# Kernel optimization log

Measured on AMD Instinct MI355X. Metric: run time of the kernel, lower is better.

The kernel has to match this reference:

```python
import jax, jax.numpy as jnp
import numpy as np

EPS = 1e-5
SCALE = 4


def _conv(x, w, b=None, stride=1, pad=0):
    y = jax.lax.conv_general_dilated(
        x, w, (stride, stride), ((pad, pad), (pad, pad)),
        dimension_numbers=("NCHW", "OIHW", "NCHW"))
    if b is not None:
        y = y + b[None, :, None, None]
    return y


def _bn(x, g, b, m, v):
    # inference-mode BatchNorm2d with running stats
    scale = g / jnp.sqrt(v + EPS)
    return (x - m[None, :, None, None]) * scale[None, :, None, None] + b[None, :, None, None]


def setup_inputs() -> dict:
    key = jax.random.key(0)
    ks = jax.random.split(key, 20)
    B, H, W = 2, 112, 256
    d = {}
    d["patch"] = jax.random.normal(ks[0], (B, 3, SCALE * H, SCALE * W), jnp.float32)
    d["disp"] = jax.random.normal(ks[1], (B, 1, H, W), jnp.float32)
    # encode: conv(3->256, k=s=4, no bias) + BN + ReLU + conv(256->256, k3 p1, no bias) + BN + ReLU
    d["w_enc1"] = jax.random.normal(ks[2], (256, 3, SCALE, SCALE), jnp.float32) * 0.05
    d["bn1_g"] = jax.random.uniform(ks[3], (256,), jnp.float32) + 0.5
    d["bn1_b"] = jax.random.normal(ks[4], (256,), jnp.float32) * 0.01
    d["bn1_m"] = jax.random.normal(ks[5], (256,), jnp.float32) * 0.01
    d["bn1_v"] = jax.random.uniform(ks[6], (256,), jnp.float32) + 0.5
    d["w_enc2"] = jax.random.normal(ks[7], (256, 256, 3, 3), jnp.float32) * 0.02
    d["bn2_g"] = jax.random.uniform(ks[8], (256,), jnp.float32) + 0.5
    d["bn2_b"] = jax.random.normal(ks[9], (256,), jnp.float32) * 0.01
    d["bn2_m"] = jax.random.normal(ks[10], (256,), jnp.float32) * 0.01
    d["bn2_v"] = jax.random.uniform(ks[11], (256,), jnp.float32) + 0.5
    # conv_disp_feat: conv(257->256, k3 p1) + ReLU + conv(256->512, k3 p1) + ReLU + conv(512->144, k1)
    d["w_c1"] = jax.random.normal(ks[12], (256, 257, 3, 3), jnp.float32) * 0.02
    d["b_c1"] = jax.random.normal(ks[13], (256,), jnp.float32) * 0.01
    d["w_c2"] = jax.random.normal(ks[14], (512, 256, 3, 3), jnp.float32) * 0.02
    d["b_c2"] = jax.random.normal(ks[15], (512,), jnp.float32) * 0.01
    d["w_c3"] = jax.random.normal(ks[16], (SCALE * SCALE * 9, 512, 1, 1), jnp.float32) * 0.02
    d["b_c3"] = jax.random.normal(ks[17], (SCALE * SCALE * 9,), jnp.float32) * 0.01
    return d


def reference(patch, disp, w_enc1, bn1_g, bn1_b, bn1_m, bn1_v,
              w_enc2, bn2_g, bn2_b, bn2_m, bn2_v,
              w_c1, b_c1, w_c2, b_c2, w_c3, b_c3):
    B, _, H, W = disp.shape
    # encoder
    feat = jax.nn.relu(_bn(_conv(patch, w_enc1, stride=SCALE), bn1_g, bn1_b, bn1_m, bn1_v))
    feat = jax.nn.relu(_bn(_conv(feat, w_enc2, pad=1), bn2_g, bn2_b, bn2_m, bn2_v))
    # mask prediction
    x = jnp.concatenate([disp, feat], axis=1)  # (B, 257, H, W)
    x = jax.nn.relu(_conv(x, w_c1, b_c1, pad=1))
    x = jax.nn.relu(_conv(x, w_c2, b_c2, pad=1))
    raw_mask = _conv(x, w_c3, b_c3)  # (B, 144, H, W)
    mask = raw_mask.reshape(B, 1, 9, SCALE, SCALE, H, W)
    mask = jax.nn.softmax(mask, axis=2)
    # F.unfold(disp, k=3, p=1): gather 3x3 neighborhoods, order (ky, kx)
    padd = jnp.pad(disp, ((0, 0), (0, 0), (1, 1), (1, 1)))
    neigh = jnp.stack([padd[:, :, ky:ky + H, kx:kx + W]
                       for ky in range(3) for kx in range(3)], axis=2)  # (B,1,9,H,W)
    up = (mask * neigh[:, :, :, None, None, :, :]).sum(axis=2)  # (B,1,s,s,H,W)
    up = up.transpose(0, 1, 4, 2, 5, 3).reshape(B, 1, SCALE * H, SCALE * W)
    return up
```

## Files before the change

kernel.cpp:

```cpp
#include <hip/hip_runtime.h>
#include <hip/hip_bf16.h>

constexpr int B_ = 2;
constexpr int H_ = 112;
constexpr int W_ = 256;
constexpr int HW_ = H_ * W_;
constexpr int PH_ = 448;
constexpr int PW_ = 1024;
constexpr float EPS_ = 1e-5f;

typedef __bf16 bf16x8 __attribute__((ext_vector_type(8)));
typedef float f32x4 __attribute__((ext_vector_type(4)));

__device__ __forceinline__ bf16x8 ld_bf16x8(const __hip_bfloat16* p) {
    return *reinterpret_cast<const bf16x8*>(p);
}
__device__ __forceinline__ bf16x8 zero_bf16x8() {
    union { int4 i; bf16x8 v; } u;
    u.i = make_int4(0, 0, 0, 0);
    return u.v;
}
__device__ __forceinline__ void gload_lds16(const __hip_bfloat16* g, __hip_bfloat16* lds) {
    __builtin_amdgcn_global_load_lds(
        (const __attribute__((address_space(1))) void*)g,
        (__attribute__((address_space(3))) void*)lds, 16, 0, 0);
}

__global__ void prep_w3_pack(const float* __restrict__ w, int COUT, int CSRC, int COFF,
                             const float* __restrict__ g, const float* __restrict__ vvar,
                             __hip_bfloat16* __restrict__ dst) {
    int idx = blockIdx.x * 256 + threadIdx.x;
    int CF = COUT / 16;
    int n = 9 * 8 * CF * 512;
    if (idx >= n) return;
    int j = idx & 7;
    int lane = (idx >> 3) & 63;
    int rest = idx >> 9;
    int cf = rest % CF;
    int rest2 = rest / CF;
    int ks = rest2 & 7;
    int tap = rest2 >> 3;
    int cout = cf * 16 + (lane & 15);
    int ci = ks * 32 + (lane >> 4) * 8 + j;
    float sc = g ? g[cout] * rsqrtf(vvar[cout] + EPS_) : 1.f;
    dst[idx] = __float2bfloat16(w[((size_t)cout * CSRC + ci + COFF) * 9 + tap] * sc);
}

__global__ void prep_c3_pack(const float* __restrict__ w, __hip_bfloat16* __restrict__ dst) {
    int idx = blockIdx.x * 256 + threadIdx.x;
    if (idx >= 16 * 9 * 512) return;
    int j = idx & 7;
    int lane = (idx >> 3) & 63;
    int rest = idx >> 9;
    int mf = rest % 9;
    int ks = rest / 9;
    int row = mf * 16 + (lane & 15);
    int ci = ks * 32 + (lane >> 4) * 8 + j;
    dst[idx] = __float2bfloat16(w[(size_t)row * 512 + ci]);
}

__global__ void prep_misc_kernel(const float* __restrict__ w_c1,
                                 const float* __restrict__ g, const float* __restrict__ bb,
                                 const float* __restrict__ m, const float* __restrict__ v,
                                 float* __restrict__ wd_c1, float* __restrict__ bias2) {
    int idx = blockIdx.x * 256 + threadIdx.x;
    if (idx < 256 * 9) {
        int co = idx / 9, tap = idx % 9;
        wd_c1[idx] = w_c1[(size_t)co * 257 * 9 + tap];
    } else if (idx < 256 * 9 + 256) {
        int co = idx - 256 * 9;
        float sc = g[co] * rsqrtf(v[co] + EPS_);
        bias2[co] = bb[co] - m[co] * sc;
    }
}

__global__ __launch_bounds__(256) void enc1_nhwc_kernel(
    const float* __restrict__ patch, const float* __restrict__ wgt,
    const float* __restrict__ g, const float* __restrict__ bb,
    const float* __restrict__ m, const float* __restrict__ v,
    __hip_bfloat16* __restrict__ out) {
    const int tid = threadIdx.x;
    const int px = tid & 63;
    const int wid = tid >> 6;
    const int bx = blockIdx.x;
    const int w0 = (bx & 3) * 64;
    const int h = bx >> 2;
    const int b = blockIdx.z;
    const int w = w0 + px;

    float p[3][4][4];
#pragma unroll
    for (int c = 0; c < 3; ++c)
#pragma unroll
        for (int ky = 0; ky < 4; ++ky) {
            float4 f = *reinterpret_cast<const float4*>(
                patch + (((size_t)b * 3 + c) * PH_ + 4 * h + ky) * PW_ + 4 * w);
            p[c][ky][0] = f.x; p[c][ky][1] = f.y; p[c][ky][2] = f.z; p[c][ky][3] = f.w;
        }

    __shared__ __hip_bfloat16 s[64][258];

    const int kbase = __builtin_amdgcn_readfirstlane(wid * 64);
    for (int i = 0; i < 64; ++i) {
        int k = kbase + i;
        const float* wk = wgt + (size_t)k * 48;
        float acc = 0.f;
#pragma unroll
        for (int c = 0; c < 3; ++c)
#pragma unroll
            for (int ky = 0; ky < 4; ++ky)
#pragma unroll
                for (int kx = 0; kx < 4; ++kx)
                    acc += p[c][ky][kx] * wk[(c * 4 + ky) * 4 + kx];
        float sc = g[k] * rsqrtf(v[k] + EPS_);
        float o = fmaxf(acc * sc + (bb[k] - m[k] * sc), 0.f);
        s[px][k] = __float2bfloat16(o);
    }
    __syncthreads();
    const size_t base = (((size_t)b * H_ + h) * W_ + w0) * 256;
    for (int j = tid; j < 64 * 128; j += 256) {
        int elem = j * 2;
        int pp = elem >> 8;
        int k = elem & 255;
        unsigned int val = *reinterpret_cast<const unsigned int*>(&s[pp][k]);
        *reinterpret_cast<unsigned int*>(out + base + elem) = val;
    }
}

template <int COUT, bool HAS_DISP>
__global__ __launch_bounds__(256, 4) void conv3x3_sb(
    const __hip_bfloat16* __restrict__ in,
    const __hip_bfloat16* __restrict__ wPack,
    const float* __restrict__ bias,
    const float* __restrict__ disp,
    const float* __restrict__ wd,
    __hip_bfloat16* __restrict__ out) {
    constexpr int CIN = 256;
    constexpr int CF = COUT / 16;
    const int tid = threadIdx.x;
    const int lane = tid & 63;
    const int wid = tid >> 6;
    const int wm = wid & 1;
    const int wn = wid >> 1;
    const int lr = lane & 15;
    const int lg = lane >> 4;

    const int bx = blockIdx.x;
    const int w0 = (bx & 1) * 128;
    const int h = bx >> 1;
    const int coutBase = blockIdx.y * 128;
    const int b = blockIdx.z;

    const int coutW = coutBase + wm * 64;
    const int cfW = coutW >> 4;
    const int pxW = wn * 64;

    __shared__ __hip_bfloat16 sIn[3][130][32];

    f32x4 acc[4][4] = {};

    const __hip_bfloat16* inb = in + (size_t)b * HW_ * CIN;
    const __hip_bfloat16* wBase = wPack + (size_t)cfW * 512 + (size_t)lane * 8;

    auto STAGE = [&](int c0) {
#pragma unroll
        for (int i = 0; i < 6; ++i) {
            const int idx = wid * 6 + i;
            const int row = idx >> 3, grp = idx & 7;
            const int y = h + row - 1;
            __hip_bfloat16* ldsb = &sIn[row][1 + grp * 16][0];
            if ((unsigned)y < (unsigned)H_) {
                const __hip_bfloat16* gp = inb +
                    ((size_t)y * W_ + w0 + grp * 16 + (lane >> 2)) * CIN + c0 + (lane & 3) * 8;
                gload_lds16(gp, ldsb);
            } else {
                *reinterpret_cast<int4*>(reinterpret_cast<char*>(ldsb) + lane * 16) =
                    make_int4(0, 0, 0, 0);
            }
        }
        if (tid < 24) {
            const int row = tid >> 3, p2 = (tid >> 2) & 1, sub = tid & 3;
            const int pxl = p2 ? 129 : 0;
            const int y = h + row - 1, x = w0 + pxl - 1;
            bf16x8 v = zero_bf16x8();
            if ((unsigned)y < (unsigned)H_ && (unsigned)x < (unsigned)W_)
                v = ld_bf16x8(inb + ((size_t)y * W_ + x) * CIN + c0 + sub * 8);
            *reinterpret_cast<bf16x8*>(&sIn[row][pxl][sub * 8]) = v;
        }
    };

    for (int ks = 0; ks < 8; ++ks) {
        STAGE(ks * 32);
        __syncthreads();
#pragma unroll
        for (int tap = 0; tap < 9; ++tap) {
            const int ky = tap / 3, kx = tap % 3;
            bf16x8 a[4];
#pragma unroll
            for (int mf = 0; mf < 4; ++mf)
                a[mf] = ld_bf16x8(wBase + ((size_t)(tap * 8 + ks) * CF + mf) * 512);
            bf16x8 bv[4];
#pragma unroll
            for (int nf = 0; nf < 4; ++nf)
                bv[nf] = *reinterpret_cast<const bf16x8*>(
                    &sIn[ky][pxW + nf * 16 + lr + kx][lg * 8]);
            __builtin_amdgcn_s_setprio(1);
#pragma unroll
            for (int nf = 0; nf < 4; ++nf)
#pragma unroll
                for (int mf = 0; mf < 4; ++mf)
                    acc[mf][nf] = __builtin_amdgcn_mfma_f32_16x16x32_bf16(
                        a[mf], bv[nf], acc[mf][nf], 0, 0, 0);
            __builtin_amdgcn_s_setprio(0);
        }
        __syncthreads();
    }

    const size_t rowBase = ((size_t)b * H_ + h) * W_;
#pragma unroll
    for (int nf = 0; nf < 4; ++nf) {
        const int px = w0 + pxW + nf * 16 + lr;
        float dnb[9];
        if (HAS_DISP) {
#pragma unroll
            for (int t = 0; t < 9; ++t) {
                int yy = h + t / 3 - 1, xx = px + t % 3 - 1;
                dnb[t] = ((unsigned)yy < (unsigned)H_ && (unsigned)xx < (unsigned)W_)
                             ? disp[((size_t)b * H_ + yy) * W_ + xx]
                             : 0.f;
            }
        }
#pragma unroll
        for (int mf = 0; mf < 4; ++mf) {
            alignas(8) __hip_bfloat16 ov[4];
#pragma unroll
            for (int r = 0; r < 4; ++r) {
                const int cout = coutW + mf * 16 + lg * 4 + r;
                float o = acc[mf][nf][r] + bias[cout];
                if (HAS_DISP) {
                    float s = 0.f;
#pragma unroll
                    for (int t = 0; t < 9; ++t) s += wd[cout * 9 + t] * dnb[t];
                    o += s;
                }
                ov[r] = __float2bfloat16(fmaxf(o, 0.f));
            }
            *reinterpret_cast<uint2*>(out + (rowBase + px) * COUT + coutW + mf * 16 + lg * 4) =
                *reinterpret_cast<const uint2*>(ov);
        }
    }
}

__global__ __launch_bounds__(256) void c3_fused_kernel(
    const __hip_bfloat16* __restrict__ x2,
    const __hip_bfloat16* __restrict__ wPack,
    const float* __restrict__ bias,
    const float* __restrict__ disp,
    float* __restrict__ outp) {
    const int tid = threadIdx.x;
    const int lane = tid & 63;
    const int wid = tid >> 6;
    const int lr = lane & 15;
    const int lg = lane >> 4;
    const int bx = blockIdx.x;
    const int w0 = (bx & 3) * 64;
    const int h = bx >> 2;
    const int b = blockIdx.z;
    const int pxw = w0 + wid * 16 + lr;

    f32x4 acc[9] = {};
    const __hip_bfloat16* inp = x2 + (((size_t)b * H_ + h) * W_ + pxw) * 512;
    const __hip_bfloat16* wl = wPack + (size_t)lane * 8;
#pragma unroll 4
    for (int ks = 0; ks < 16; ++ks) {
        const int c0 = ks * 32 + lg * 8;
        bf16x8 bv = ld_bf16x8(inp + c0);
#pragma unroll
        for (int mf = 0; mf < 9; ++mf) {
            bf16x8 av = ld_bf16x8(wl + ((size_t)ks * 9 + mf) * 512);
            acc[mf] = __builtin_amdgcn_mfma_f32_16x16x32_bf16(av, bv, acc[mf], 0, 0, 0);
        }
    }

    float dnb[9];
#pragma unroll
    for (int t = 0; t < 9; ++t) {
        int yy = h + t / 3 - 1, xx = pxw + t % 3 - 1;
        dnb[t] = ((unsigned)yy < (unsigned)H_ && (unsigned)xx < (unsigned)W_)
                     ? disp[((size_t)b * H_ + yy) * W_ + xx]
                     : 0.f;
    }
    float oo[4];
#pragma unroll
    for (int r = 0; r < 4; ++r) {
        const int st = lg * 4 + r;
        float sv[9], mx = -1e30f;
#pragma unroll
        for (int mf = 0; mf < 9; ++mf) {
            sv[mf] = acc[mf][r] + bias[mf * 16 + st];
            mx = fmaxf(mx, sv[mf]);
        }
        float sum = 0.f, wsum = 0.f;
#pragma unroll
        for (int mf = 0; mf < 9; ++mf) {
            float e = __expf(sv[mf] - mx);
            sum += e;
            wsum += e * dnb[mf];
        }
        oo[r] = wsum / sum;
    }
    float4 o4 = make_float4(oo[0], oo[1], oo[2], oo[3]);
    *reinterpret_cast<float4*>(outp + ((size_t)b * PH_ + 4 * h + lg) * PW_ + 4 * pxw) = o4;
}

extern "C" void kernel_launch(void* const* d_in, const int* in_sizes, int n_in,
                              void* d_out, int out_size, void* d_ws, size_t ws_size,
                              hipStream_t stream) {
    const float* patch = (const float*)d_in[0];
    const float* disp = (const float*)d_in[1];
    const float* w_enc1 = (const float*)d_in[2];
    const float* bn1_g = (const float*)d_in[3];
    const float* bn1_b = (const float*)d_in[4];
    const float* bn1_m = (const float*)d_in[5];
    const float* bn1_v = (const float*)d_in[6];
    const float* w_enc2 = (const float*)d_in[7];
    const float* bn2_g = (const float*)d_in[8];
    const float* bn2_b = (const float*)d_in[9];
    const float* bn2_m = (const float*)d_in[10];
    const float* bn2_v = (const float*)d_in[11];
    const float* w_c1 = (const float*)d_in[12];
    const float* b_c1 = (const float*)d_in[13];
    const float* w_c2 = (const float*)d_in[14];
    const float* b_c2 = (const float*)d_in[15];
    const float* w_c3 = (const float*)d_in[16];
    const float* b_c3 = (const float*)d_in[17];
    float* out = (float*)d_out;

    char* ws = (char*)d_ws;
    const size_t S1 = (size_t)B_ * HW_ * 256 * sizeof(__hip_bfloat16);
    const size_t S2 = (size_t)B_ * HW_ * 512 * sizeof(__hip_bfloat16);
    __hip_bfloat16* feat1 = (__hip_bfloat16*)ws;   ws += S1;
    __hip_bfloat16* feat2 = (__hip_bfloat16*)ws;   ws += S1;
    __hip_bfloat16* x1    = (__hip_bfloat16*)ws;   ws += S1;
    __hip_bfloat16* x2    = (__hip_bfloat16*)ws;   ws += S2;
    __hip_bfloat16* wP_enc2 = (__hip_bfloat16*)ws; ws += (size_t)9 * 256 * 256 * 2;
    __hip_bfloat16* wP_c1   = (__hip_bfloat16*)ws; ws += (size_t)9 * 256 * 256 * 2;
    __hip_bfloat16* wP_c2   = (__hip_bfloat16*)ws; ws += (size_t)9 * 512 * 256 * 2;
    __hip_bfloat16* wP_c3   = (__hip_bfloat16*)ws; ws += (size_t)16 * 9 * 512 * 2;
    float* bias2 = (float*)ws;                     ws += 256 * 4;
    float* wd_c1 = (float*)ws;                     ws += 256 * 9 * 4;

    dim3 blk(256, 1, 1);

    prep_w3_pack<<<dim3((9 * 256 * 256 + 255) / 256), blk, 0, stream>>>(
        w_enc2, 256, 256, 0, bn2_g, bn2_v, wP_enc2);
    prep_w3_pack<<<dim3((9 * 256 * 256 + 255) / 256), blk, 0, stream>>>(
        w_c1, 256, 257, 1, nullptr, nullptr, wP_c1);
    prep_w3_pack<<<dim3((9 * 512 * 256 + 255) / 256), blk, 0, stream>>>(
        w_c2, 512, 256, 0, nullptr, nullptr, wP_c2);
    prep_c3_pack<<<dim3((16 * 9 * 512 + 255) / 256), blk, 0, stream>>>(w_c3, wP_c3);
    prep_misc_kernel<<<dim3((256 * 9 + 256 + 255) / 256), blk, 0, stream>>>(
        w_c1, bn2_g, bn2_b, bn2_m, bn2_v, wd_c1, bias2);

    enc1_nhwc_kernel<<<dim3(H_ * 4, 1, B_), blk, 0, stream>>>(
        patch, w_enc1, bn1_g, bn1_b, bn1_m, bn1_v, feat1);
    conv3x3_sb<256, false><<<dim3(2 * H_, 2, B_), blk, 0, stream>>>(
        feat1, wP_enc2, bias2, nullptr, nullptr, feat2);
    conv3x3_sb<256, true><<<dim3(2 * H_, 2, B_), blk, 0, stream>>>(
        feat2, wP_c1, b_c1, disp, wd_c1, x1);
    conv3x3_sb<512, false><<<dim3(2 * H_, 4, B_), blk, 0, stream>>>(
        x1, wP_c2, b_c2, nullptr, nullptr, x2);
    c3_fused_kernel<<<dim3(H_ * 4, 1, B_), blk, 0, stream>>>(
        x2, wP_c3, b_c3, disp, out);
}
```

Measured before the change: 387.2 us.

## Double-buffer LDS input tiles and software-pipeline weight loads in conv3x3

The 3x3 conv kernel now double-buffers the shared input tile. It issues the next K-slice's global-to-LDS loads while the current slice's MFMAs run, and prefetches the weight fragments several taps ahead in registers. This leaves one barrier per K step instead of two and hides global load latency behind compute. It also remaps the block index so that spatially adjacent blocks are interleaved across the grid, and lowers the launch-bounds occupancy hint from 4 to 3 to give the extra registers room, at the cost of fewer resident waves.

```diff
diff --git a/kernel.cpp b/kernel.cpp
--- a/kernel.cpp
+++ b/kernel.cpp
@@ -128,7 +128,7 @@
 }
 
 template <int COUT, bool HAS_DISP>
-__global__ __launch_bounds__(256, 4) void conv3x3_sb(
+__global__ __launch_bounds__(256, 3) void conv3x3_pl(
     const __hip_bfloat16* __restrict__ in,
     const __hip_bfloat16* __restrict__ wPack,
     const float* __restrict__ bias,
@@ -145,7 +145,8 @@
     const int lr = lane & 15;
     const int lg = lane >> 4;
 
-    const int bx = blockIdx.x;
+    int bx = blockIdx.x;
+    bx = (bx & 7) * 28 + (bx >> 3);
     const int w0 = (bx & 1) * 128;
     const int h = bx >> 1;
     const int coutBase = blockIdx.y * 128;
@@ -155,20 +156,23 @@
     const int cfW = coutW >> 4;
     const int pxW = wn * 64;
 
-    __shared__ __hip_bfloat16 sIn[3][130][32];
+    __shared__ __hip_bfloat16 sIn[2][3][130][32];
 
     f32x4 acc[4][4] = {};
 
     const __hip_bfloat16* inb = in + (size_t)b * HW_ * CIN;
     const __hip_bfloat16* wBase = wPack + (size_t)cfW * 512 + (size_t)lane * 8;
 
-    auto STAGE = [&](int c0) {
+    const int t_row = tid >> 3, t_p2 = (tid >> 2) & 1, t_sub = tid & 3;
+    const int t_pxl = t_p2 ? 129 : 0;
+
+    auto STAGE_G = [&](int buf, int c0) {
 #pragma unroll
         for (int i = 0; i < 6; ++i) {
             const int idx = wid * 6 + i;
             const int row = idx >> 3, grp = idx & 7;
             const int y = h + row - 1;
-            __hip_bfloat16* ldsb = &sIn[row][1 + grp * 16][0];
+            __hip_bfloat16* ldsb = &sIn[buf][row][1 + grp * 16][0];
             if ((unsigned)y < (unsigned)H_) {
                 const __hip_bfloat16* gp = inb +
                     ((size_t)y * W_ + w0 + grp * 16 + (lane >> 2)) * CIN + c0 + (lane & 3) * 8;
@@ -178,41 +182,70 @@
                     make_int4(0, 0, 0, 0);
             }
         }
-        if (tid < 24) {
-            const int row = tid >> 3, p2 = (tid >> 2) & 1, sub = tid & 3;
-            const int pxl = p2 ? 129 : 0;
-            const int y = h + row - 1, x = w0 + pxl - 1;
-            bf16x8 v = zero_bf16x8();
-            if ((unsigned)y < (unsigned)H_ && (unsigned)x < (unsigned)W_)
-                v = ld_bf16x8(inb + ((size_t)y * W_ + x) * CIN + c0 + sub * 8);
-            *reinterpret_cast<bf16x8*>(&sIn[row][pxl][sub * 8]) = v;
-        }
     };
+    auto TAIL_LOAD = [&](int c0) -> bf16x8 {
+        const int y = h + t_row - 1, x = w0 + t_pxl - 1;
+        bf16x8 v = zero_bf16x8();
+        if ((unsigned)y < (unsigned)H_ && (unsigned)x < (unsigned)W_)
+            v = ld_bf16x8(inb + ((size_t)y * W_ + x) * CIN + c0 + t_sub * 8);
+        return v;
+    };
+
+    auto LD_A = [&](int tap, int kss, bf16x8* dst) {
+#pragma unroll
+        for (int mf = 0; mf < 4; ++mf)
+            dst[mf] = ld_bf16x8(wBase + ((size_t)(tap * 8 + kss) * CF + mf) * 512);
+    };
+    auto DO_TAP = [&](int tap, const bf16x8* a, int cur) {
+        const int ky = tap / 3, kx = tap % 3;
+        bf16x8 bv[4];
+#pragma unroll
+        for (int nf = 0; nf < 4; ++nf)
+            bv[nf] = *reinterpret_cast<const bf16x8*>(
+                &sIn[cur][ky][pxW + nf * 16 + lr + kx][lg * 8]);
+        __builtin_amdgcn_s_setprio(1);
+#pragma unroll
+        for (int nf = 0; nf < 4; ++nf)
+#pragma unroll
+            for (int mf = 0; mf < 4; ++mf)
+                acc[mf][nf] = __builtin_amdgcn_mfma_f32_16x16x32_bf16(
+                    a[mf], bv[nf], acc[mf][nf], 0, 0, 0);
+        __builtin_amdgcn_s_setprio(0);
+    };
+
+    STAGE_G(0, 0);
+    if (tid < 24) {
+        bf16x8 t0 = TAIL_LOAD(0);
+        *reinterpret_cast<bf16x8*>(&sIn[0][t_row][t_pxl][t_sub * 8]) = t0;
+    }
+    bf16x8 A0[4];
+    LD_A(0, 0, A0);
+    __syncthreads();
 
     for (int ks = 0; ks < 8; ++ks) {
-        STAGE(ks * 32);
-        __syncthreads();
-#pragma unroll
-        for (int tap = 0; tap < 9; ++tap) {
-            const int ky = tap / 3, kx = tap % 3;
-            bf16x8 a[4];
-#pragma unroll
-            for (int mf = 0; mf < 4; ++mf)
-                a[mf] = ld_bf16x8(wBase + ((size_t)(tap * 8 + ks) * CF + mf) * 512);
-            bf16x8 bv[4];
-#pragma unroll
-            for (int nf = 0; nf < 4; ++nf)
-                bv[nf] = *reinterpret_cast<const bf16x8*>(
-                    &sIn[ky][pxW + nf * 16 + lr + kx][lg * 8]);
-            __builtin_amdgcn_s_setprio(1);
-#pragma unroll
-            for (int nf = 0; nf < 4; ++nf)
-#pragma unroll
-                for (int mf = 0; mf < 4; ++mf)
-                    acc[mf][nf] = __builtin_amdgcn_mfma_f32_16x16x32_bf16(
-                        a[mf], bv[nf], acc[mf][nf], 0, 0, 0);
-            __builtin_amdgcn_s_setprio(0);
-        }
+        const int cur = ks & 1;
+        const bool nxt = ks < 7;
+        const int ksn = nxt ? ks + 1 : 7;
+        bf16x8 tnext = zero_bf16x8();
+        if (tid < 24 && nxt) tnext = TAIL_LOAD(ksn * 32);
+        bf16x8 A1[4], A2[4];
+        LD_A(1, ks, A1);
+        LD_A(2, ks, A2);
+        __builtin_amdgcn_sched_barrier(0);
+        if (nxt) STAGE_G(cur ^ 1, ksn * 32);
+        __builtin_amdgcn_sched_barrier(0);
+        bf16x8 A3[4], A4[4], A5[4], A6[4], A7[4], A8[4];
+        DO_TAP(0, A0, cur);  LD_A(3, ks, A3);
+        DO_TAP(1, A1, cur);  LD_A(4, ks, A4);
+        DO_TAP(2, A2, cur);  LD_A(5, ks, A5);
+        DO_TAP(3, A3, cur);  LD_A(6, ks, A6);
+        DO_TAP(4, A4, cur);  LD_A(7, ks, A7);
+        DO_TAP(5, A5, cur);  LD_A(8, ks, A8);
+        DO_TAP(6, A6, cur);  LD_A(0, ksn, A0);
+        DO_TAP(7, A7, cur);
+        DO_TAP(8, A8, cur);
+        if (tid < 24 && nxt)
+            *reinterpret_cast<bf16x8*>(&sIn[cur ^ 1][t_row][t_pxl][t_sub * 8]) = tnext;
         __syncthreads();
     }
 
@@ -364,11 +397,11 @@
 
     enc1_nhwc_kernel<<<dim3(H_ * 4, 1, B_), blk, 0, stream>>>(
         patch, w_enc1, bn1_g, bn1_b, bn1_m, bn1_v, feat1);
-    conv3x3_sb<256, false><<<dim3(2 * H_, 2, B_), blk, 0, stream>>>(
+    conv3x3_pl<256, false><<<dim3(2 * H_, 2, B_), blk, 0, stream>>>(
         feat1, wP_enc2, bias2, nullptr, nullptr, feat2);
-    conv3x3_sb<256, true><<<dim3(2 * H_, 2, B_), blk, 0, stream>>>(
+    conv3x3_pl<256, true><<<dim3(2 * H_, 2, B_), blk, 0, stream>>>(
         feat2, wP_c1, b_c1, disp, wd_c1, x1);
-    conv3x3_sb<512, false><<<dim3(2 * H_, 4, B_), blk, 0, stream>>>(
+    conv3x3_pl<512, false><<<dim3(2 * H_, 4, B_), blk, 0, stream>>>(
         x1, wP_c2, b_c2, nullptr, nullptr, x2);
     c3_fused_kernel<<<dim3(H_ * 4, 1, B_), blk, 0, stream>>>(
         x2, wP_c3, b_c3, disp, out);
```

After: 384.3 us. Within noise of the previous version (-0.8%).

## Widen conv3x3 blocks to full rows with swizzled LDS and row remap

Applied to the files above, without the earlier changes.

The 3x3 conv kernel now uses 512-thread blocks that each cover a full 256-pixel image row instead of half a row. This removes the halo loads between half-row tiles and reuses each staged input row across more warps. LDS reads and writes use an XOR swizzle on the 16-byte channel group to avoid bank conflicts. Block indices are remapped so neighbouring rows are spread across blocks. The cost is fewer blocks (half the grid) and higher per-block LDS and register demand, and the launch_bounds of 512 threads with min 4 blocks may be hard to satisfy.

```diff
diff --git a/kernel.cpp b/kernel.cpp
--- a/kernel.cpp
+++ b/kernel.cpp
@@ -128,7 +128,7 @@
 }
 
 template <int COUT, bool HAS_DISP>
-__global__ __launch_bounds__(256, 4) void conv3x3_sb(
+__global__ __launch_bounds__(512, 4) void conv3x3_wide(
     const __hip_bfloat16* __restrict__ in,
     const __hip_bfloat16* __restrict__ wPack,
     const float* __restrict__ bias,
@@ -145,9 +145,8 @@
     const int lr = lane & 15;
     const int lg = lane >> 4;
 
-    const int bx = blockIdx.x;
-    const int w0 = (bx & 1) * 128;
-    const int h = bx >> 1;
+    int bx = blockIdx.x;
+    const int h = (bx & 7) * 14 + (bx >> 3);
     const int coutBase = blockIdx.y * 128;
     const int b = blockIdx.z;
 
@@ -155,46 +154,56 @@
     const int cfW = coutW >> 4;
     const int pxW = wn * 64;
 
-    __shared__ __hip_bfloat16 sIn[3][130][32];
+    __shared__ __hip_bfloat16 sIn[3][260][32];
 
     f32x4 acc[4][4] = {};
 
     const __hip_bfloat16* inb = in + (size_t)b * HW_ * CIN;
     const __hip_bfloat16* wBase = wPack + (size_t)cfW * 512 + (size_t)lane * 8;
 
+    const int key0 = (lr >> 1) & 3;
+    const int key1 = ((lr + 1) >> 1) & 3;
+    const int key2 = (key0 + 1) & 3;
+    const int loff0 = lr * 64 + ((lg ^ key0) << 4);
+    const int loff1 = lr * 64 + ((lg ^ key1) << 4);
+    const int loff2 = lr * 64 + ((lg ^ key2) << 4);
+
+    const int key_w = (((lane >> 2) + 1) >> 1) & 3;
+    const int csw = (((lane & 3) ^ key_w)) * 8;
+
+    if (tid < 24) {
+        const int row = tid >> 3, p2 = (tid >> 2) & 1, sub = tid & 3;
+        const int pxl = p2 ? 257 : 0;
+        *reinterpret_cast<bf16x8*>(&sIn[row][pxl][sub * 8]) = zero_bf16x8();
+    }
+
     auto STAGE = [&](int c0) {
 #pragma unroll
         for (int i = 0; i < 6; ++i) {
             const int idx = wid * 6 + i;
-            const int row = idx >> 3, grp = idx & 7;
+            const int row = idx >> 4, grp = idx & 15;
             const int y = h + row - 1;
             __hip_bfloat16* ldsb = &sIn[row][1 + grp * 16][0];
             if ((unsigned)y < (unsigned)H_) {
                 const __hip_bfloat16* gp = inb +
-                    ((size_t)y * W_ + w0 + grp * 16 + (lane >> 2)) * CIN + c0 + (lane & 3) * 8;
+                    ((size_t)y * W_ + grp * 16 + (lane >> 2)) * CIN + c0 + csw;
                 gload_lds16(gp, ldsb);
             } else {
                 *reinterpret_cast<int4*>(reinterpret_cast<char*>(ldsb) + lane * 16) =
                     make_int4(0, 0, 0, 0);
             }
         }
-        if (tid < 24) {
-            const int row = tid >> 3, p2 = (tid >> 2) & 1, sub = tid & 3;
-            const int pxl = p2 ? 129 : 0;
-            const int y = h + row - 1, x = w0 + pxl - 1;
-            bf16x8 v = zero_bf16x8();
-            if ((unsigned)y < (unsigned)H_ && (unsigned)x < (unsigned)W_)
-                v = ld_bf16x8(inb + ((size_t)y * W_ + x) * CIN + c0 + sub * 8);
-            *reinterpret_cast<bf16x8*>(&sIn[row][pxl][sub * 8]) = v;
-        }
     };
 
+    constexpr int ROWB = 260 * 32 * 2;
     for (int ks = 0; ks < 8; ++ks) {
         STAGE(ks * 32);
         __syncthreads();
+        const char* sB = reinterpret_cast<const char*>(&sIn[0][0][0]) + pxW * 64;
 #pragma unroll
         for (int tap = 0; tap < 9; ++tap) {
             const int ky = tap / 3, kx = tap % 3;
+            const int lofk = (kx == 0) ? loff0 : (kx == 1) ? loff1 : loff2;
             bf16x8 a[4];
 #pragma unroll
             for (int mf = 0; mf < 4; ++mf)
@@ -203,7 +212,7 @@
 #pragma unroll
             for (int nf = 0; nf < 4; ++nf)
                 bv[nf] = *reinterpret_cast<const bf16x8*>(
-                    &sIn[ky][pxW + nf * 16 + lr + kx][lg * 8]);
+                    sB + ky * ROWB + (nf * 16 + kx) * 64 + lofk);
             __builtin_amdgcn_s_setprio(1);
 #pragma unroll
             for (int nf = 0; nf < 4; ++nf)
@@ -219,7 +228,7 @@
     const size_t rowBase = ((size_t)b * H_ + h) * W_;
 #pragma unroll
     for (int nf = 0; nf < 4; ++nf) {
-        const int px = w0 + pxW + nf * 16 + lr;
+        const int px = pxW + nf * 16 + lr;
         float dnb[9];
         if (HAS_DISP) {
 #pragma unroll
@@ -351,6 +360,7 @@
     float* wd_c1 = (float*)ws;                     ws += 256 * 9 * 4;
 
     dim3 blk(256, 1, 1);
+    dim3 blk2(512, 1, 1);
 
     prep_w3_pack<<<dim3((9 * 256 * 256 + 255) / 256), blk, 0, stream>>>(
         w_enc2, 256, 256, 0, bn2_g, bn2_v, wP_enc2);
@@ -364,11 +374,11 @@
 
     enc1_nhwc_kernel<<<dim3(H_ * 4, 1, B_), blk, 0, stream>>>(
         patch, w_enc1, bn1_g, bn1_b, bn1_m, bn1_v, feat1);
-    conv3x3_sb<256, false><<<dim3(2 * H_, 2, B_), blk, 0, stream>>>(
+    conv3x3_wide<256, false><<<dim3(H_, 2, B_), blk2, 0, stream>>>(
         feat1, wP_enc2, bias2, nullptr, nullptr, feat2);
-    conv3x3_sb<256, true><<<dim3(2 * H_, 2, B_), blk, 0, stream>>>(
+    conv3x3_wide<256, true><<<dim3(H_, 2, B_), blk2, 0, stream>>>(
         feat2, wP_c1, b_c1, disp, wd_c1, x1);
-    conv3x3_sb<512, false><<<dim3(2 * H_, 4, B_), blk, 0, stream>>>(
+    conv3x3_wide<512, false><<<dim3(H_, 4, B_), blk2, 0, stream>>>(
         x1, wP_c2, b_c2, nullptr, nullptr, x2);
     c3_fused_kernel<<<dim3(H_ * 4, 1, B_), blk, 0, stream>>>(
         x2, wP_c3, b_c3, disp, out);
```

New measurement: 375.9 us. -2.9%, faster.
